# Kernel optimization log

Hardware: AMD Instinct MI355X
Metric: run time of the kernel (lower is better)

## Reference

```python
import jax, jax.numpy as jnp
import numpy as np

SUPPORT = 10
NEIGHBOR_NUM = 20
DEGREE = 8
NEG_SLOPE = 0.2
EPS = 1e-12


def _norm(x, axis):
    n = jnp.linalg.norm(x, axis=axis, keepdims=True)
    return x / jnp.maximum(n, EPS)


def knn_index(v, k):
    # v: (b, n, 3) -> (b, n, k) indices of k nearest (self excluded)
    inner = jnp.einsum('bnd,bmd->bnm', v, v)
    quad = jnp.sum(v * v, axis=2)
    dist = quad[:, :, None] - 2.0 * inner + quad[:, None, :]
    _, idx = jax.lax.top_k(-dist, k + 1)  # smallest distances
    return idx[:, :, 1:]


def gather_nb(feat, idx):
    # feat (b,n,c), idx (b,n,k) -> (b,n,k,c)
    b = feat.shape[0]
    return feat[jnp.arange(b)[:, None, None], idx]


def nb_dir_norm(vertices, idx):
    nb = gather_nb(vertices, idx) - vertices[:, :, None, :]
    return _norm(nb, axis=-1)


def op3d(idx, vertices, directions, kernel_num):
    # Conv_surface: directions (3, support*kernel)
    ndn = nb_dir_norm(vertices, idx)                 # (b,n,k,3)
    sdn = _norm(directions, axis=0)
    theta = jax.nn.relu(jnp.einsum('bnkd,de->bnke', ndn, sdn))
    b, n, kk, _ = theta.shape
    theta = theta.reshape(b, n, kk, SUPPORT, kernel_num)
    return jnp.sum(jnp.max(theta, axis=2), axis=2)    # (b,n,kernel)


def opnd(idx, vertices, feat, w, bias, directions, out_ch):
    # Conv_layer: w (in,(s+1)*out), bias ((s+1)*out), directions (3, s*out)
    ndn = nb_dir_norm(vertices, idx)
    sdn = _norm(directions, axis=0)
    theta = jax.nn.relu(jnp.einsum('bnkd,de->bnke', ndn, sdn))  # (b,n,k,s*out)
    fo = feat @ w + bias                                        # (b,n,(s+1)*out)
    fc = fo[:, :, :out_ch]
    fs = gather_nb(fo[:, :, out_ch:], idx)                      # (b,n,k,s*out)
    b, n, kk, _ = theta.shape
    act = (theta * fs).reshape(b, n, kk, SUPPORT, out_ch)
    return fc + jnp.sum(jnp.max(act, axis=2), axis=2)


def tree_gcn(x, w_root, w_branch, w_l1, w_l2, bias, activation):
    # depth-0 upsampling TreeGCN: x (b,node,in) -> (b,node*DEGREE,out)
    b, node, in_f = x.shape
    root = x @ w_root                                           # (b,node,out)
    br = jax.nn.leaky_relu(jnp.einsum('bni,nij->bnj', x, w_branch), NEG_SLOPE)
    br = br.reshape(b, node * DEGREE, in_f)
    br = (br @ w_l1) @ w_l2                                     # (b,node*deg,out)
    out = jnp.repeat(root, DEGREE, axis=1) + br
    if activation:
        out = jax.nn.leaky_relu(out + jnp.tile(bias, (1, node, 1)), NEG_SLOPE)
    return out


def setup_inputs() -> dict:
    key = jax.random.key(0)
    ks = iter(jax.random.split(key, 32))
    r = lambda shape: (jax.random.normal(next(ks), shape, dtype=jnp.float32) * 0.1)
    inp = {
        'coase_points': jax.random.normal(next(ks), (2, 512, 3), dtype=jnp.float32),
        'd0': r((3, SUPPORT * 32)),
        'w1': r((32, (SUPPORT + 1) * 64)), 'b1': r(((SUPPORT + 1) * 64,)), 'dir1': r((3, SUPPORT * 64)),
        'd2': r((3, SUPPORT * 32)),
        'w3': r((32, (SUPPORT + 1) * 64)), 'b3': r(((SUPPORT + 1) * 64,)), 'dir3': r((3, SUPPORT * 64)),
        'w4': r((64, (SUPPORT + 1) * 64)), 'b4': r(((SUPPORT + 1) * 64,)), 'dir4': r((3, SUPPORT * 64)),
        'w5': r((64, (SUPPORT + 1) * 64)), 'b5': r(((SUPPORT + 1) * 64,)), 'dir5': r((3, SUPPORT * 64)),
        'root1': r((64, 3)), 'branch1': r((512, 64, DEGREE * 64)),
        'loop1a': r((64, 64 * SUPPORT)), 'loop1b': r((64 * SUPPORT, 3)), 'bias1': r((1, DEGREE, 3)),
        'root2': r((64, 3)), 'branch2': r((4096, 64, DEGREE * 64)),
        'loop2a': r((64, 64 * SUPPORT)), 'loop2b': r((64 * SUPPORT, 3)),
    }
    return inp


def reference(coase_points, d0, w1, b1, dir1, d2, w3, b3, dir3, w4, b4, dir4,
              w5, b5, dir5, root1, branch1, loop1a, loop1b, bias1,
              root2, branch2, loop2a, loop2b):
    idx = knn_index(coase_points, NEIGHBOR_NUM)
    fm0 = jax.nn.relu(op3d(idx, coase_points, d0, 32))  # dropout is identity in eval
    fm1 = jax.nn.relu(opnd(idx, coase_points, fm0, w1, b1, dir1, 64))
    pc1 = tree_gcn(fm1, root1, branch1, loop1a, loop1b, bias1, True)   # (b, 4096, 3)
    idx2 = knn_index(pc1, NEIGHBOR_NUM)
    fm2 = jax.nn.relu(op3d(idx2, pc1, d2, 32))
    fm3 = jax.nn.relu(opnd(idx2, pc1, fm2, w3, b3, dir3, 64))
    fm4 = jax.nn.relu(opnd(idx2, pc1, fm3, w4, b4, dir4, 64))
    fm5 = jax.nn.relu(opnd(idx2, pc1, fm4, w5, b5, dir5, 64))
    pc2 = tree_gcn(fm5, root2, branch2, loop2a, loop2b, None, False)   # (b, 32768, 3)
    return pc1, pc2
```

## Files before the change

kernel.cpp:

```cpp
#include <hip/hip_runtime.h>
#include <hip/hip_bf16.h>
#include <stdint.h>

#define SUPPORT 10
#define KNN 20
#define DEGREE 8

__global__ __launch_bounds__(256) void prep_kernel(
    const float* __restrict__ d0, const float* __restrict__ dir1,
    const float* __restrict__ d2, const float* __restrict__ dir3,
    const float* __restrict__ dir4, const float* __restrict__ dir5,
    float* __restrict__ sdn0, float* __restrict__ sdn1, float* __restrict__ sdn2,
    float* __restrict__ sdn3, float* __restrict__ sdn4, float* __restrict__ sdn5,
    const float* __restrict__ l1a, const float* __restrict__ l1b,
    const float* __restrict__ l2a, const float* __restrict__ l2b,
    float* __restrict__ wc1, float* __restrict__ wc2) {
#pragma clang fp contract(off)
  if (blockIdx.x < 13) {
    int t = blockIdx.x * 256 + threadIdx.x;
    if (t >= 3200) return;
    const float* src; float* dst; int cols; int e;
    if (t < 320)       { src = d0;   dst = sdn0; cols = 320; e = t; }
    else if (t < 960)  { src = dir1; dst = sdn1; cols = 640; e = t - 320; }
    else if (t < 1280) { src = d2;   dst = sdn2; cols = 320; e = t - 960; }
    else if (t < 1920) { src = dir3; dst = sdn3; cols = 640; e = t - 1280; }
    else if (t < 2560) { src = dir4; dst = sdn4; cols = 640; e = t - 1920; }
    else               { src = dir5; dst = sdn5; cols = 640; e = t - 2560; }
    float a = src[e], b = src[cols + e], c = src[2 * cols + e];
    float nrm = sqrtf(a * a + b * b + c * c);
    nrm = fmaxf(nrm, 1e-12f);
    dst[e] = a / nrm; dst[cols + e] = b / nrm; dst[2 * cols + e] = c / nrm;
  } else {
    int which = blockIdx.x - 13;
    int tt = threadIdx.x;
    if (tt >= 192) return;
    const float* A  = which ? l2a : l1a;
    const float* Bm = which ? l2b : l1b;
    float* out = which ? wc2 : wc1;
    int i = tt / 3, c = tt % 3;
    float s = 0.f;
    for (int k = 0; k < 640; ++k) s = fmaf(A[i * 640 + k], Bm[k * 3 + c], s);
    out[i * 3 + c] = s;
  }
}

template <int MPER, int WAVES>
__global__ __launch_bounds__(WAVES * 64) void knn_kernel(const float* __restrict__ pts,
                                                         int N, int* __restrict__ idx_out) {
#pragma clang fp contract(off)
  extern __shared__ uint32_t kbuf[];
  int w = threadIdx.x >> 6, lane = threadIdx.x & 63;
  int g = blockIdx.x * WAVES + w;
  int b = g / N, n = g % N;
  volatile uint32_t* K = kbuf + (size_t)w * 64 * MPER;
  const float* pb = pts + (size_t)b * N * 3;

  float nx = pb[n * 3], ny = pb[n * 3 + 1], nz = pb[n * 3 + 2];
  float qn = nx * nx + ny * ny + nz * nz;

  unsigned long long mymin = ~0ull;
  for (int j = 0; j < MPER; ++j) {
    int m = j * 64 + lane;
    float mx = pb[m * 3], my = pb[m * 3 + 1], mz = pb[m * 3 + 2];
    float inner = nx * mx + ny * my + nz * mz;
    float qm = mx * mx + my * my + mz * mz;
    float d = (qn - 2.0f * inner) + qm;
    uint32_t u = __float_as_uint(d);
    u ^= (u & 0x80000000u) ? 0xFFFFFFFFu : 0x80000000u;
    K[lane * MPER + (j ^ (lane & (MPER - 1)))] = u;
    unsigned long long key = ((unsigned long long)u << 32) | (unsigned)m;
    mymin = key < mymin ? key : mymin;
  }
  for (int r = 0; r < 21; ++r) {
    unsigned long long best = mymin;
#pragma unroll
    for (int s = 1; s < 64; s <<= 1) {
      unsigned long long o = __shfl_xor(best, s, 64);
      best = o < best ? o : best;
    }
    unsigned m = (unsigned)best;
    if (r > 0 && lane == 0) idx_out[(size_t)g * KNN + (r - 1)] = (int)m;
    if (r == 20) break;
    int owner = m & 63, slot = m >> 6;
    if (lane == slot) K[owner * MPER + (slot ^ (owner & (MPER - 1)))] = 0xFFFFFFFFu;
    unsigned long long cand = ~0ull;
    if (lane < MPER) {
      uint32_t v = K[owner * MPER + (lane ^ (owner & (MPER - 1)))];
      cand = ((unsigned long long)v << 32) | (unsigned)(lane * 64 + owner);
    }
#pragma unroll
    for (int s = 1; s < 64; s <<= 1) {
      unsigned long long o = __shfl_xor(cand, s, 64);
      cand = o < cand ? o : cand;
    }
    if (lane == owner) mymin = cand;
  }
}

__global__ __launch_bounds__(256) void ndn_kernel(const float* __restrict__ pts,
                                                  const int* __restrict__ idx,
                                                  float* __restrict__ ndn, int N) {
#pragma clang fp contract(off)
  int t = blockIdx.x * 256 + threadIdx.x;
  int total = 2 * N * KNN;
  if (t >= total) return;
  int k = t % KNN, g = t / KNN;
  int b = g / N, n = g % N;
  int m = idx[(size_t)g * KNN + k];
  const float* pb = pts + (size_t)b * N * 3;
  float dx = pb[m * 3] - pb[n * 3];
  float dy = pb[m * 3 + 1] - pb[n * 3 + 1];
  float dz = pb[m * 3 + 2] - pb[n * 3 + 2];
  float nr = sqrtf(dx * dx + dy * dy + dz * dz);
  nr = fmaxf(nr, 1e-12f);
  ndn[(size_t)t * 3] = dx / nr; ndn[(size_t)t * 3 + 1] = dy / nr; ndn[(size_t)t * 3 + 2] = dz / nr;
}

__global__ __launch_bounds__(256) void op3d_kernel(const float* __restrict__ ndn,
                                                   const float* __restrict__ sdn,
                                                   float* __restrict__ out, int N) {
#pragma clang fp contract(off)
  int c = threadIdx.x & 31;
  int g = (blockIdx.x * 256 + threadIdx.x) >> 5;
  if (g >= 2 * N) return;
  const float* nd = ndn + (size_t)g * 60;
  float sv0[SUPPORT], sv1[SUPPORT], sv2[SUPPORT], mm[SUPPORT];
#pragma unroll
  for (int s = 0; s < SUPPORT; ++s) {
    sv0[s] = sdn[s * 32 + c];
    sv1[s] = sdn[320 + s * 32 + c];
    sv2[s] = sdn[640 + s * 32 + c];
    mm[s] = 0.f;
  }
  for (int k = 0; k < KNN; ++k) {
    float nx = nd[k * 3], ny = nd[k * 3 + 1], nz = nd[k * 3 + 2];
#pragma unroll
    for (int s = 0; s < SUPPORT; ++s) {
      float t = nx * sv0[s] + ny * sv1[s] + nz * sv2[s];
      mm[s] = fmaxf(mm[s], t);
    }
  }
  float acc = 0.f;
#pragma unroll
  for (int s = 0; s < SUPPORT; ++s) acc += mm[s];
  out[(size_t)g * 32 + c] = acc;
}

template <int K>
__global__ __launch_bounds__(256) void fo_kernel(const float* __restrict__ feat,
                                                 const float* __restrict__ wmat,
                                                 const float* __restrict__ bias,
                                                 float* __restrict__ fo, int N) {
  __shared__ float fL[8 * K];
  int t = threadIdx.x;
  int gbase = blockIdx.x * 8;
  for (int i = t; i < 8 * K; i += 256) fL[i] = feat[(size_t)gbase * K + i];
  __syncthreads();
  float a0[8], a1[8], a2[8];
#pragma unroll
  for (int gg = 0; gg < 8; ++gg) { a0[gg] = 0.f; a1[gg] = 0.f; a2[gg] = 0.f; }
  bool has3 = (t < 192);
  for (int i = 0; i < K; ++i) {
    float w0 = wmat[i * 704 + t];
    float w1 = wmat[i * 704 + t + 256];
    float w2 = has3 ? wmat[i * 704 + t + 512] : 0.f;
#pragma unroll
    for (int gg = 0; gg < 8; ++gg) {
      float f = fL[gg * K + i];
      a0[gg] = fmaf(f, w0, a0[gg]);
      a1[gg] = fmaf(f, w1, a1[gg]);
      a2[gg] = fmaf(f, w2, a2[gg]);
    }
  }
  float b0 = bias[t], b1 = bias[t + 256], b2 = has3 ? bias[t + 512] : 0.f;
#pragma unroll
  for (int gg = 0; gg < 8; ++gg) {
    size_t base = (size_t)(gbase + gg) * 704;
    fo[base + t] = a0[gg] + b0;
    fo[base + t + 256] = a1[gg] + b1;
    if (has3) fo[base + t + 512] = a2[gg] + b2;
  }
}

__global__ __launch_bounds__(256) void opnd_kernel(const float* __restrict__ ndn,
                                                   const int* __restrict__ idx,
                                                   const float* __restrict__ fo,
                                                   const float* __restrict__ sdn,
                                                   float* __restrict__ fm, int N) {
#pragma clang fp contract(off)
  __shared__ float ndL[4][64];
  __shared__ int offL[4][24];
  int w = threadIdx.x >> 6, lane = threadIdx.x & 63;
  int g = blockIdx.x * 4 + w;
  if (lane < 60) ndL[w][lane] = ndn[(size_t)g * 60 + lane];
  if (lane < KNN) offL[w][lane] = ((g / N) * N + idx[(size_t)g * KNN + lane]) * 704 + 64;
  __syncthreads();
  const float* ndw = ndL[w];
  const int* offw = offL[w];
  float sv0[SUPPORT], sv1[SUPPORT], sv2[SUPPORT], mm[SUPPORT];
#pragma unroll
  for (int s = 0; s < SUPPORT; ++s) {
    sv0[s] = sdn[s * 64 + lane];
    sv1[s] = sdn[640 + s * 64 + lane];
    sv2[s] = sdn[1280 + s * 64 + lane];
    mm[s] = -__builtin_inff();
  }
  for (int k = 0; k < KNN; ++k) {
    float nx = ndw[k * 3], ny = ndw[k * 3 + 1], nz = ndw[k * 3 + 2];
    int off = offw[k];
#pragma unroll
    for (int s = 0; s < SUPPORT; ++s) {
      float t = fmaxf(nx * sv0[s] + ny * sv1[s] + nz * sv2[s], 0.f);
      float f = fo[(size_t)off + s * 64 + lane];
      mm[s] = fmaxf(mm[s], t * f);
    }
  }
  float acc = 0.f;
#pragma unroll
  for (int s = 0; s < SUPPORT; ++s) acc += mm[s];
  float fc = fo[(size_t)g * 704 + lane];
  float v = fc + acc;
  fm[(size_t)g * 64 + lane] = fmaxf(v, 0.f);
}

__global__ __launch_bounds__(256) void tree_exact_kernel(
    const float* __restrict__ x, const float* __restrict__ wroot,
    const float* __restrict__ wb, const float* __restrict__ l1,
    const float* __restrict__ l2, const float* __restrict__ bias,
    float* __restrict__ out, int node) {
  __shared__ float xL[2][64];
  __shared__ float brL[2][512];
  __shared__ float tL[4][640];
  __shared__ float rootv[2][3];
  int n = blockIdx.x, t = threadIdx.x;
  if (t < 128) xL[t >> 6][t & 63] = x[(size_t)(t >> 6) * node * 64 + (size_t)n * 64 + (t & 63)];
  __syncthreads();
  {
#pragma clang fp contract(off)
    const float* wrow = wb + (size_t)n * 64 * 512;
    int j0 = 2 * t;
    float a00 = 0.f, a01 = 0.f, a10 = 0.f, a11 = 0.f;
    for (int i = 0; i < 64; ++i) {
      float w0 = wrow[(size_t)i * 512 + j0];
      float w1 = wrow[(size_t)i * 512 + j0 + 1];
      float f0 = xL[0][i], f1 = xL[1][i];
      a00 = a00 + f0 * w0; a01 = a01 + f0 * w1;
      a10 = a10 + f1 * w0; a11 = a11 + f1 * w1;
    }
    brL[0][j0]     = a00 >= 0.f ? a00 : 0.2f * a00;
    brL[0][j0 + 1] = a01 >= 0.f ? a01 : 0.2f * a01;
    brL[1][j0]     = a10 >= 0.f ? a10 : 0.2f * a10;
    brL[1][j0 + 1] = a11 >= 0.f ? a11 : 0.2f * a11;
  }
  if (t < 6) {
    int b = t / 3, c = t % 3;
    float r = 0.f;
    for (int i = 0; i < 64; ++i) r = fmaf(xL[b][i], wroot[i * 3 + c], r);
    rootv[b][c] = r;
  }
  __syncthreads();
  for (int chunk = 0; chunk < 4; ++chunk) {
    for (int e = t; e < 4 * 640; e += 256) {
      int q = e / 640, j = e % 640;
      int p = chunk * 4 + q, b = p >> 3, d = p & 7;
      float acc = 0.f;
      for (int i = 0; i < 64; ++i)
        acc = fmaf(brL[b][d * 64 + i], l1[i * 640 + j], acc);
      tL[q][j] = acc;
    }
    __syncthreads();
    if (t < 12) {
      int q = t / 3, c = t % 3;
      int p = chunk * 4 + q, b = p >> 3, d = p & 7;
      float s = 0.f;
      for (int j = 0; j < 640; ++j) s = fmaf(tL[q][j], l2[j * 3 + c], s);
      float v = rootv[b][c] + s;
      v = v + bias[d * 3 + c];
      v = v >= 0.f ? v : 0.2f * v;
      out[((size_t)b * node * DEGREE + (size_t)n * DEGREE + d) * 3 + c] = v;
    }
    __syncthreads();
  }
}

__global__ __launch_bounds__(256) void tree_kernel(const float* __restrict__ x,
                                                   const float* __restrict__ wroot,
                                                   const float* __restrict__ wb,
                                                   const float* __restrict__ wc,
                                                   float* __restrict__ out,
                                                   int node) {
  __shared__ float xL[2][64];
  __shared__ float brL[2][512];
  int n = blockIdx.x;
  int t = threadIdx.x;
  if (t < 128) xL[t >> 6][t & 63] = x[(size_t)(t >> 6) * node * 64 + (size_t)n * 64 + (t & 63)];
  __syncthreads();
  float a00 = 0.f, a01 = 0.f, a10 = 0.f, a11 = 0.f;
  const float* wrow = wb + (size_t)n * 64 * 512;
  int j0 = 2 * t;
  for (int i = 0; i < 64; ++i) {
    float2 wv = *(const float2*)(wrow + (size_t)i * 512 + j0);
    float f0 = xL[0][i], f1 = xL[1][i];
    a00 += f0 * wv.x; a01 += f0 * wv.y;
    a10 += f1 * wv.x; a11 += f1 * wv.y;
  }
  brL[0][j0]     = a00 >= 0.f ? a00 : 0.2f * a00;
  brL[0][j0 + 1] = a01 >= 0.f ? a01 : 0.2f * a01;
  brL[1][j0]     = a10 >= 0.f ? a10 : 0.2f * a10;
  brL[1][j0 + 1] = a11 >= 0.f ? a11 : 0.2f * a11;
  __syncthreads();
  if (t < 48) {
    int b = t / 24, rem = t % 24, d = rem / 3, c = rem % 3;
    float root = 0.f, brs = 0.f;
    for (int i = 0; i < 64; ++i) {
      root = fmaf(xL[b][i], wroot[i * 3 + c], root);
      brs  = fmaf(brL[b][d * 64 + i], wc[i * 3 + c], brs);
    }
    float v = root + brs;
    out[((size_t)b * node * DEGREE + (size_t)n * DEGREE + d) * 3 + c] = v;
  }
}

extern "C" void kernel_launch(void* const* d_in, const int* in_sizes, int n_in,
                              void* d_out, int out_size, void* d_ws, size_t ws_size,
                              hipStream_t stream) {
  const float* pts1    = (const float*)d_in[0];
  const float* d0      = (const float*)d_in[1];
  const float* w1      = (const float*)d_in[2];
  const float* b1      = (const float*)d_in[3];
  const float* dir1    = (const float*)d_in[4];
  const float* d2      = (const float*)d_in[5];
  const float* w3      = (const float*)d_in[6];
  const float* b3      = (const float*)d_in[7];
  const float* dir3    = (const float*)d_in[8];
  const float* w4      = (const float*)d_in[9];
  const float* b4      = (const float*)d_in[10];
  const float* dir4    = (const float*)d_in[11];
  const float* w5      = (const float*)d_in[12];
  const float* b5      = (const float*)d_in[13];
  const float* dir5    = (const float*)d_in[14];
  const float* root1   = (const float*)d_in[15];
  const float* branch1 = (const float*)d_in[16];
  const float* l1a     = (const float*)d_in[17];
  const float* l1b     = (const float*)d_in[18];
  const float* bias1   = (const float*)d_in[19];
  const float* root2   = (const float*)d_in[20];
  const float* branch2 = (const float*)d_in[21];
  const float* l2a     = (const float*)d_in[22];
  const float* l2b     = (const float*)d_in[23];

  float* ws = (float*)d_ws;
  size_t o = 0;
  float* sdn0 = ws + o; o += 960;
  float* sdn1 = ws + o; o += 1920;
  float* sdn2 = ws + o; o += 960;
  float* sdn3 = ws + o; o += 1920;
  float* sdn4 = ws + o; o += 1920;
  float* sdn5 = ws + o; o += 1920;
  float* wc1  = ws + o; o += 192;
  float* wc2  = ws + o; o += 192;
  int*   idxb = (int*)(ws + o); o += (size_t)2 * 4096 * KNN;
  float* ndnb = ws + o; o += (size_t)2 * 4096 * KNN * 3;
  float* fo   = ws + o; o += (size_t)2 * 4096 * 704;
  float* fmA  = ws + o; o += (size_t)2 * 4096 * 64;
  float* fmB  = ws + o; o += (size_t)2 * 4096 * 64;

  float* pc1 = (float*)d_out;
  float* pc2 = (float*)d_out + 2 * 4096 * 3;

  prep_kernel<<<15, 256, 0, stream>>>(d0, dir1, d2, dir3, dir4, dir5,
                                      sdn0, sdn1, sdn2, sdn3, sdn4, sdn5,
                                      l1a, l1b, l2a, l2b, wc1, wc2);

  knn_kernel<8, 4><<<2 * 512 / 4, 256, 4 * 64 * 8 * 4, stream>>>(pts1, 512, idxb);
  ndn_kernel<<<(2 * 512 * KNN + 255) / 256, 256, 0, stream>>>(pts1, idxb, ndnb, 512);
  op3d_kernel<<<2 * 512 * 32 / 256, 256, 0, stream>>>(ndnb, sdn0, fmA, 512);
  fo_kernel<32><<<2 * 512 / 8, 256, 0, stream>>>(fmA, w1, b1, fo, 512);
  opnd_kernel<<<2 * 512 / 4, 256, 0, stream>>>(ndnb, idxb, fo, sdn1, fmB, 512);
  tree_exact_kernel<<<512, 256, 0, stream>>>(fmB, root1, branch1, l1a, l1b,
                                             bias1, pc1, 512);

  knn_kernel<64, 2><<<2 * 4096 / 2, 128, 2 * 64 * 64 * 4, stream>>>(pc1, 4096, idxb);
  ndn_kernel<<<(2 * 4096 * KNN + 255) / 256, 256, 0, stream>>>(pc1, idxb, ndnb, 4096);
  op3d_kernel<<<2 * 4096 * 32 / 256, 256, 0, stream>>>(ndnb, sdn2, fmA, 4096);
  fo_kernel<32><<<2 * 4096 / 8, 256, 0, stream>>>(fmA, w3, b3, fo, 4096);
  opnd_kernel<<<2 * 4096 / 4, 256, 0, stream>>>(ndnb, idxb, fo, sdn3, fmB, 4096);
  fo_kernel<64><<<2 * 4096 / 8, 256, 0, stream>>>(fmB, w4, b4, fo, 4096);
  opnd_kernel<<<2 * 4096 / 4, 256, 0, stream>>>(ndnb, idxb, fo, sdn4, fmA, 4096);
  fo_kernel<64><<<2 * 4096 / 8, 256, 0, stream>>>(fmA, w5, b5, fo, 4096);
  opnd_kernel<<<2 * 4096 / 4, 256, 0, stream>>>(ndnb, idxb, fo, sdn5, fmB, 4096);
  tree_kernel<<<4096, 256, 0, stream>>>(fmB, root2, branch2, wc2, pc2, 4096);
}
```

Before: 692.1 us.

## Convert points to SoA for knn loads and flatten tree_exact chunk loop

Adds small kernels that turn the xyz point arrays into separate x/y/z buffers, so the knn distance loop reads coalesced unit-stride data instead of stride-3 loads. It also rewrites tree_exact_kernel to compute all 16 intermediate rows into a larger shared buffer in one pass. That pass needs a single barrier, and 48 threads then finish the projection, replacing four chunked rounds with repeated syncs. The cost is one extra kernel launch and much more shared memory per block, which may reduce occupancy.

```diff
diff --git a/kernel.cpp b/kernel.cpp
--- a/kernel.cpp
+++ b/kernel.cpp
@@ -14,7 +14,9 @@
     float* __restrict__ sdn3, float* __restrict__ sdn4, float* __restrict__ sdn5,
     const float* __restrict__ l1a, const float* __restrict__ l1b,
     const float* __restrict__ l2a, const float* __restrict__ l2b,
-    float* __restrict__ wc1, float* __restrict__ wc2) {
+    float* __restrict__ wc1, float* __restrict__ wc2,
+    const float* __restrict__ pts1,
+    float* __restrict__ px1, float* __restrict__ py1, float* __restrict__ pz1) {
 #pragma clang fp contract(off)
   if (blockIdx.x < 13) {
     int t = blockIdx.x * 256 + threadIdx.x;
@@ -30,7 +32,7 @@
     float nrm = sqrtf(a * a + b * b + c * c);
     nrm = fmaxf(nrm, 1e-12f);
     dst[e] = a / nrm; dst[cols + e] = b / nrm; dst[2 * cols + e] = c / nrm;
-  } else {
+  } else if (blockIdx.x < 15) {
     int which = blockIdx.x - 13;
     int tt = threadIdx.x;
     if (tt >= 192) return;
@@ -41,27 +43,47 @@
     float s = 0.f;
     for (int k = 0; k < 640; ++k) s = fmaf(A[i * 640 + k], Bm[k * 3 + c], s);
     out[i * 3 + c] = s;
-  }
+  } else {
+    int t = (blockIdx.x - 15) * 256 + threadIdx.x;
+    if (t >= 1024) return;
+    px1[t] = pts1[t * 3];
+    py1[t] = pts1[t * 3 + 1];
+    pz1[t] = pts1[t * 3 + 2];
+  }
+}
+
+__global__ __launch_bounds__(256) void soa2_kernel(const float* __restrict__ pc1,
+                                                   float* __restrict__ px,
+                                                   float* __restrict__ py,
+                                                   float* __restrict__ pz) {
+  int t = blockIdx.x * 256 + threadIdx.x;
+  if (t >= 8192) return;
+  px[t] = pc1[t * 3];
+  py[t] = pc1[t * 3 + 1];
+  pz[t] = pc1[t * 3 + 2];
 }
 
 template <int MPER, int WAVES>
-__global__ __launch_bounds__(WAVES * 64) void knn_kernel(const float* __restrict__ pts,
-                                                         int N, int* __restrict__ idx_out) {
+__global__ __launch_bounds__(WAVES * 64) void knn_kernel(
+    const float* __restrict__ px, const float* __restrict__ py,
+    const float* __restrict__ pz, int N, int* __restrict__ idx_out) {
 #pragma clang fp contract(off)
   extern __shared__ uint32_t kbuf[];
   int w = threadIdx.x >> 6, lane = threadIdx.x & 63;
   int g = blockIdx.x * WAVES + w;
   int b = g / N, n = g % N;
   volatile uint32_t* K = kbuf + (size_t)w * 64 * MPER;
-  const float* pb = pts + (size_t)b * N * 3;
-
-  float nx = pb[n * 3], ny = pb[n * 3 + 1], nz = pb[n * 3 + 2];
+  const float* PX = px + (size_t)b * N;
+  const float* PY = py + (size_t)b * N;
+  const float* PZ = pz + (size_t)b * N;
+
+  float nx = PX[n], ny = PY[n], nz = PZ[n];
   float qn = nx * nx + ny * ny + nz * nz;
 
   unsigned long long mymin = ~0ull;
   for (int j = 0; j < MPER; ++j) {
     int m = j * 64 + lane;
-    float mx = pb[m * 3], my = pb[m * 3 + 1], mz = pb[m * 3 + 2];
+    float mx = PX[m], my = PY[m], mz = PZ[m];
     float inner = nx * mx + ny * my + nz * mz;
     float qm = mx * mx + my * my + mz * mz;
     float d = (qn - 2.0f * inner) + qm;
@@ -228,15 +250,15 @@
     const float* __restrict__ wb, const float* __restrict__ l1,
     const float* __restrict__ l2, const float* __restrict__ bias,
     float* __restrict__ out, int node) {
+#pragma clang fp contract(off)
   __shared__ float xL[2][64];
   __shared__ float brL[2][512];
-  __shared__ float tL[4][640];
+  __shared__ float tL[16][640];
   __shared__ float rootv[2][3];
   int n = blockIdx.x, t = threadIdx.x;
   if (t < 128) xL[t >> 6][t & 63] = x[(size_t)(t >> 6) * node * 64 + (size_t)n * 64 + (t & 63)];
   __syncthreads();
   {
-#pragma clang fp contract(off)
     const float* wrow = wb + (size_t)n * 64 * 512;
     int j0 = 2 * t;
     float a00 = 0.f, a01 = 0.f, a10 = 0.f, a11 = 0.f;
@@ -259,27 +281,25 @@
     rootv[b][c] = r;
   }
   __syncthreads();
-  for (int chunk = 0; chunk < 4; ++chunk) {
-    for (int e = t; e < 4 * 640; e += 256) {
-      int q = e / 640, j = e % 640;
-      int p = chunk * 4 + q, b = p >> 3, d = p & 7;
-      float acc = 0.f;
-      for (int i = 0; i < 64; ++i)
-        acc = fmaf(brL[b][d * 64 + i], l1[i * 640 + j], acc);
-      tL[q][j] = acc;
-    }
-    __syncthreads();
-    if (t < 12) {
-      int q = t / 3, c = t % 3;
-      int p = chunk * 4 + q, b = p >> 3, d = p & 7;
-      float s = 0.f;
-      for (int j = 0; j < 640; ++j) s = fmaf(tL[q][j], l2[j * 3 + c], s);
-      float v = rootv[b][c] + s;
-      v = v + bias[d * 3 + c];
-      v = v >= 0.f ? v : 0.2f * v;
-      out[((size_t)b * node * DEGREE + (size_t)n * DEGREE + d) * 3 + c] = v;
-    }
-    __syncthreads();
+#pragma unroll 4
+  for (int u = 0; u < 40; ++u) {
+    int e = u * 256 + t;
+    int p = e / 640, j = e % 640;
+    const float* brow = brL[p >> 3] + (p & 7) * 64;
+    float acc = 0.f;
+    for (int i = 0; i < 64; ++i)
+      acc = fmaf(brow[i], l1[i * 640 + j], acc);
+    tL[p][j] = acc;
+  }
+  __syncthreads();
+  if (t < 48) {
+    int p = t / 3, c = t % 3, b = p >> 3, d = p & 7;
+    float s = 0.f;
+    for (int j = 0; j < 640; ++j) s = fmaf(tL[p][j], l2[j * 3 + c], s);
+    float v = rootv[b][c] + s;
+    v = v + bias[d * 3 + c];
+    v = v >= 0.f ? v : 0.2f * v;
+    out[((size_t)b * node * DEGREE + (size_t)n * DEGREE + d) * 3 + c] = v;
   }
 }
 
@@ -359,6 +379,12 @@
   float* sdn5 = ws + o; o += 1920;
   float* wc1  = ws + o; o += 192;
   float* wc2  = ws + o; o += 192;
+  float* px1  = ws + o; o += 1024;
+  float* py1  = ws + o; o += 1024;
+  float* pz1  = ws + o; o += 1024;
+  float* px2  = ws + o; o += 8192;
+  float* py2  = ws + o; o += 8192;
+  float* pz2  = ws + o; o += 8192;
   int*   idxb = (int*)(ws + o); o += (size_t)2 * 4096 * KNN;
   float* ndnb = ws + o; o += (size_t)2 * 4096 * KNN * 3;
   float* fo   = ws + o; o += (size_t)2 * 4096 * 704;
@@ -368,11 +394,12 @@
   float* pc1 = (float*)d_out;
   float* pc2 = (float*)d_out + 2 * 4096 * 3;
 
-  prep_kernel<<<15, 256, 0, stream>>>(d0, dir1, d2, dir3, dir4, dir5,
+  prep_kernel<<<19, 256, 0, stream>>>(d0, dir1, d2, dir3, dir4, dir5,
                                       sdn0, sdn1, sdn2, sdn3, sdn4, sdn5,
-                                      l1a, l1b, l2a, l2b, wc1, wc2);
-
-  knn_kernel<8, 4><<<2 * 512 / 4, 256, 4 * 64 * 8 * 4, stream>>>(pts1, 512, idxb);
+                                      l1a, l1b, l2a, l2b, wc1, wc2,
+                                      pts1, px1, py1, pz1);
+
+  knn_kernel<8, 4><<<2 * 512 / 4, 256, 4 * 64 * 8 * 4, stream>>>(px1, py1, pz1, 512, idxb);
   ndn_kernel<<<(2 * 512 * KNN + 255) / 256, 256, 0, stream>>>(pts1, idxb, ndnb, 512);
   op3d_kernel<<<2 * 512 * 32 / 256, 256, 0, stream>>>(ndnb, sdn0, fmA, 512);
   fo_kernel<32><<<2 * 512 / 8, 256, 0, stream>>>(fmA, w1, b1, fo, 512);
@@ -380,7 +407,8 @@
   tree_exact_kernel<<<512, 256, 0, stream>>>(fmB, root1, branch1, l1a, l1b,
                                              bias1, pc1, 512);
 
-  knn_kernel<64, 2><<<2 * 4096 / 2, 128, 2 * 64 * 64 * 4, stream>>>(pc1, 4096, idxb);
+  soa2_kernel<<<32, 256, 0, stream>>>(pc1, px2, py2, pz2);
+  knn_kernel<64, 2><<<2 * 4096 / 2, 128, 2 * 64 * 64 * 4, stream>>>(px2, py2, pz2, 4096, idxb);
   ndn_kernel<<<(2 * 4096 * KNN + 255) / 256, 256, 0, stream>>>(pc1, idxb, ndnb, 4096);
   op3d_kernel<<<2 * 4096 * 32 / 256, 256, 0, stream>>>(ndnb, sdn2, fmA, 4096);
   fo_kernel<32><<<2 * 4096 / 8, 256, 0, stream>>>(fmA, w3, b3, fo, 4096);
```

Result: faster. 671.0 us (-3.1%).
